# Kernel tuning notes

Measured on AMD Instinct MI355X. Metric: run time of the kernel, lower is better.

The kernel has to match this reference:

```python
import jax, jax.numpy as jnp
import numpy as np

EPS = 1e-08

def setup_inputs() -> dict:
    key = jax.random.key(0)
    k1, k2 = jax.random.split(key)
    h = jax.random.normal(k1, (4096, 512), dtype=jnp.float32)   # [B, D]
    A = jax.random.normal(k2, (32768, 512), dtype=jnp.float32)  # [K, D]
    return {"h": h, "A": A}

def _l2_normalize(x, eps=EPS):
    # matches torch F.normalize(p=2): x / max(||x||, eps)
    n = jnp.sqrt(jnp.sum(x * x, axis=-1, keepdims=True))
    return x / jnp.maximum(n, eps)

def reference(h, A):
    # cosine metric: normalize both, matmul, argmax over K
    h_n = _l2_normalize(h)                      # [B, D]
    A_n = _l2_normalize(A)                      # [K, D]
    scores = jnp.einsum('bd,kd->bk', h_n, A_n)  # [B, K]
    idx = jnp.argmax(scores, axis=1, keepdims=True)  # [B, 1] int
    return idx
```

## Files before the change

kernel.cpp:

```cpp
#include <hip/hip_runtime.h>
#include <stdint.h>


#define DIM 512
#define B_ROWS 4096
#define K_ROWS 32768
#define BT 128
#define KT 128
#define NKT (K_ROWS / KT)
#define KSLOTS 32
#define NCHUNK 4
#define QSCALE (127.0f / 0.26f)

typedef __attribute__((ext_vector_type(4))) float fx4;
typedef __attribute__((ext_vector_type(4))) int int4v;
typedef unsigned long long u64;

__device__ __forceinline__ uint32_t ford(float s) {
    uint32_t u = __float_as_uint(s);
    return u ^ ((uint32_t)((int32_t)u >> 31) | 0x80000000u);
}
__device__ __forceinline__ u64 umax64(u64 a, u64 b) { return a > b ? a : b; }
__device__ __forceinline__ u64 umin64(u64 a, u64 b) { return a < b ? a : b; }
__device__ __forceinline__ uint32_t umax32(uint32_t a, uint32_t b) { return a > b ? a : b; }
__device__ __forceinline__ uint32_t umin32(uint32_t a, uint32_t b) { return a < b ? a : b; }

__device__ __forceinline__ int q8(float x, float qs) {
    int v = __float2int_rn(x * qs);
    return v < -127 ? -127 : (v > 127 ? 127 : v);
}

__global__ __launch_bounds__(256) void prep_kernel(const float* __restrict__ A,
                                                   const float* __restrict__ h,
                                                   char* __restrict__ a8,
                                                   char* __restrict__ h8,
                                                   float* __restrict__ rn) {
    const int lane = threadIdx.x & 63, wid = threadIdx.x >> 6;
    const bool isA = blockIdx.x < 8192;
    const int row = (isA ? blockIdx.x : blockIdx.x - 8192) * 4 + wid;
    const float* src = (isA ? A : h) + (size_t)row * DIM;
    char* dst = (isA ? a8 : h8) + (size_t)row * DIM;

    const fx4* p = (const fx4*)src;
    fx4 a = p[lane * 2], b = p[lane * 2 + 1];
    float ss = a[0]*a[0] + a[1]*a[1] + a[2]*a[2] + a[3]*a[3]
             + b[0]*b[0] + b[1]*b[1] + b[2]*b[2] + b[3]*b[3];
    #pragma unroll
    for (int off = 32; off > 0; off >>= 1) ss += __shfl_xor(ss, off, 64);
    float r = 1.0f / fmaxf(sqrtf(ss), 1e-8f);
    if (isA && lane == 0) rn[row] = r;

    float qs = r * QSCALE;
    int v0 = q8(a[0], qs), v1 = q8(a[1], qs), v2 = q8(a[2], qs), v3 = q8(a[3], qs);
    int v4 = q8(b[0], qs), v5 = q8(b[1], qs), v6 = q8(b[2], qs), v7 = q8(b[3], qs);
    uint32_t lo = (uint32_t)(v0 & 255) | ((uint32_t)(v1 & 255) << 8)
                | ((uint32_t)(v2 & 255) << 16) | ((uint32_t)(v3 & 255) << 24);
    uint32_t hi = (uint32_t)(v4 & 255) | ((uint32_t)(v5 & 255) << 8)
                | ((uint32_t)(v6 & 255) << 16) | ((uint32_t)(v7 & 255) << 24);
    *reinterpret_cast<uint2*>(dst + lane * 8) = make_uint2(lo, hi);
}

typedef __attribute__((address_space(3))) uint32_t lds_u32;
typedef __attribute__((address_space(1))) const uint32_t g_u32;

__global__ __launch_bounds__(256, 3) void score_kernel(
    const char* __restrict__ h8, const char* __restrict__ a8,
    u64* __restrict__ cand)
{
    __shared__ __attribute__((aligned(16))) char smem[33792];
    char* hf = smem;
    char* af = smem + 16384;

    const int t = threadIdx.x, lane = t & 63, wid = t >> 6;
    const int wm = wid >> 1, wn = wid & 1;
    const int lr = lane & 15, q = lane >> 4;
    const int btile = blockIdx.x >> 5, kslot = blockIdx.x & 31;
    const int b0 = btile * BT;

    const int srow = lane >> 3;
    const int scol = (lane & 7) ^ srow;
    const int s7 = lr & 7;
    const int sw0 = (q ^ s7) * 16;
    const int sw1 = ((4 + q) ^ s7) * 16;

    const char* hsrc = h8 + (size_t)b0 * DIM;

    uint32_t v1[16], v2[16];
    #pragma unroll
    for (int s = 0; s < 16; s++) { v1[s] = 0u; v2[s] = 0u; }

    int it = 0;
    #pragma unroll 1
    for (int kt = kslot; kt < NKT; kt += KSLOTS, it++) {
        const int k0 = kt * KT;
        const char* asrc = a8 + (size_t)k0 * DIM;

        int4v acc[4][4];
        #pragma unroll
        for (int mi = 0; mi < 4; mi++)
            #pragma unroll
            for (int ni = 0; ni < 4; ni++)
                acc[mi][ni] = (int4v){0, 0, 0, 0};

        #pragma unroll 1
        for (int dc = 0; dc < NCHUNK; dc++) {
            __syncthreads();
            #pragma unroll
            for (int i = 0; i < 4; i++) {
                int issue = wid * 4 + i;
                size_t roff = (size_t)(issue * 8 + srow) * DIM + dc * 128 + scol * 16;
                __builtin_amdgcn_global_load_lds((g_u32*)(hsrc + roff),
                    (lds_u32*)(hf + issue * 1024), 16, 0, 0);
                __builtin_amdgcn_global_load_lds((g_u32*)(asrc + roff),
                    (lds_u32*)(af + issue * 1024), 16, 0, 0);
            }
            __syncthreads();

            int4v af0[4], af1[4];
            #pragma unroll
            for (int ni = 0; ni < 4; ni++) {
                const char* base = af + (wn * 64 + ni * 16 + lr) * 128;
                af0[ni] = *reinterpret_cast<const int4v*>(base + sw0);
                af1[ni] = *reinterpret_cast<const int4v*>(base + sw1);
            }
            #pragma unroll
            for (int mi = 0; mi < 4; mi++) {
                const char* base = hf + (wm * 64 + mi * 16 + lr) * 128;
                int4v h0 = *reinterpret_cast<const int4v*>(base + sw0);
                int4v h1 = *reinterpret_cast<const int4v*>(base + sw1);
                #pragma unroll
                for (int ni = 0; ni < 4; ni++) {
                    acc[mi][ni] = __builtin_amdgcn_mfma_i32_16x16x64_i8(h0, af0[ni], acc[mi][ni], 0, 0, 0);
                    acc[mi][ni] = __builtin_amdgcn_mfma_i32_16x16x64_i8(h1, af1[ni], acc[mi][ni], 0, 0, 0);
                }
            }
        }

        const uint32_t metabase = (uint32_t)(it << 2);
        #pragma unroll
        for (int mi = 0; mi < 4; mi++)
            #pragma unroll
            for (int ni = 0; ni < 4; ni++) {
                const uint32_t meta = metabase | (uint32_t)ni;
                #pragma unroll
                for (int r = 0; r < 4; r++) {
                    uint32_t ord = (uint32_t)acc[mi][ni][r] ^ 0x80000000u;
                    uint32_t pk = (ord & 0xFFFFFFC0u) | meta;
                    int s = mi * 4 + r;
                    uint32_t lo = umin32(v1[s], pk);
                    v1[s] = umax32(v1[s], pk);
                    v2[s] = umax32(v2[s], lo);
                }
            }
    }

    uint32_t* cl = (uint32_t*)smem;
    u64 g1 = 0, g2 = 0, g3 = 0;
    for (int pass = 0; pass < 2; pass++) {
        __syncthreads();
        #pragma unroll
        for (int s = 0; s < 16; s++) {
            int mi = s >> 2, r = s & 3;
            int row_local = wm * 64 + mi * 16 + q * 4 + r;
            cl[row_local * 33 + wn * 16 + lr] = pass ? v2[s] : v1[s];
        }
        __syncthreads();
        if (t < BT) {
            #pragma unroll 4
            for (int j = 0; j < 32; j++) {
                uint32_t pv = cl[t * 33 + j];
                uint32_t meta = pv & 63u;
                int k = (kslot + (int)(meta >> 2) * KSLOTS) * KT
                      + (j >> 4) * 64 + (int)(meta & 3u) * 16 + (j & 15);
                u64 e = ((u64)(pv & 0xFFFFFFC0u) << 32) | (u64)(~(uint32_t)k);
                u64 t1 = umax64(g1, e), t2 = umin64(g1, e);
                g3 = umax64(g3, umin64(g2, t2));
                g2 = umax64(g2, t2);
                g1 = t1;
            }
        }
    }
    if (t < BT) {
        size_t base = ((size_t)(b0 + t) * KSLOTS + kslot) * 3;
        cand[base] = g1;
        cand[base + 1] = g2;
        cand[base + 2] = g3;
    }
}

__global__ __launch_bounds__(256) void refine_kernel(
    const float* __restrict__ h, const float* __restrict__ A,
    const float* __restrict__ rn, const u64* __restrict__ cand,
    int* __restrict__ out)
{
    const int t = threadIdx.x, lane = t & 63, wid = t >> 6;
    const int row = blockIdx.x * 4 + wid;
    const u64* cr = cand + (size_t)row * (KSLOTS * 3);
    u64 x0 = cr[lane];
    u64 x1 = (lane < KSLOTS * 3 - 64) ? cr[64 + lane] : 0ULL;

    u64 sel[8];
    #pragma unroll
    for (int j = 0; j < 8; j++) {
        u64 v = umax64(x0, x1);
        #pragma unroll
        for (int m = 32; m >= 1; m >>= 1) v = umax64(v, __shfl_xor(v, m, 64));
        sel[j] = v;
        if (x0 == v) x0 = 0;
        else if (x1 == v) x1 = 0;
    }

    const fx4* hp = reinterpret_cast<const fx4*>(h + (size_t)row * DIM);
    fx4 h0 = hp[lane * 2], h1 = hp[lane * 2 + 1];

    u64 best = 0;
    #pragma unroll
    for (int j = 0; j < 8; j++) {
        uint32_t kg = ~(uint32_t)sel[j];
        const fx4* ap = reinterpret_cast<const fx4*>(A + (size_t)kg * DIM);
        fx4 a0 = ap[lane * 2], a1 = ap[lane * 2 + 1];
        float s = h0[0]*a0[0] + h0[1]*a0[1] + h0[2]*a0[2] + h0[3]*a0[3]
                + h1[0]*a1[0] + h1[1]*a1[1] + h1[2]*a1[2] + h1[3]*a1[3];
        #pragma unroll
        for (int m = 32; m >= 1; m >>= 1) s += __shfl_xor(s, m, 64);
        s *= rn[kg];
        u64 pk = ((u64)ford(s) << 32) | (u64)(~kg);
        best = umax64(best, pk);
    }
    if (lane == 0) out[row] = (int)(~(uint32_t)best);
}

extern "C" void kernel_launch(void* const* d_in, const int* in_sizes, int n_in,
                              void* d_out, int out_size, void* d_ws, size_t ws_size,
                              hipStream_t stream) {
    const float* h = (const float*)d_in[0];
    const float* A = (const float*)d_in[1];
    int* out = (int*)d_out;

    char* w = (char*)d_ws;
    char* a8 = w;
    char* h8 = w + (size_t)K_ROWS * DIM;
    float* rn = (float*)(w + (size_t)(K_ROWS + B_ROWS) * DIM);
    u64* cand = (u64*)(w + (size_t)(K_ROWS + B_ROWS) * DIM
                         + (size_t)K_ROWS * sizeof(float));

    prep_kernel<<<8192 + 1024, 256, 0, stream>>>(A, h, a8, h8, rn);
    score_kernel<<<32 * KSLOTS, 256, 0, stream>>>(h8, a8, cand);
    refine_kernel<<<B_ROWS / 4, 256, 0, stream>>>(h, A, rn, cand, out);
}
```

Baseline: 203.9 us.

## Double-buffer LDS tiles to overlap global loads with int8 MFMA compute

Replaces the single LDS tile buffer with two 32 KB buffers. The next D-chunk is now issued via global_load_lds into the alternate buffer while the current chunk is consumed by MFMAs, and one barrier per chunk replaces two. LDS use doubles to 64 KB, so launch bounds drop from 3 to 2 blocks per CU, trading occupancy for latency hiding. The loop is hardcoded to 8 k-tile iterations per slot.

```diff
diff --git a/kernel.cpp b/kernel.cpp
--- a/kernel.cpp
+++ b/kernel.cpp
@@ -63,13 +63,11 @@
 typedef __attribute__((address_space(3))) uint32_t lds_u32;
 typedef __attribute__((address_space(1))) const uint32_t g_u32;
 
-__global__ __launch_bounds__(256, 3) void score_kernel(
+__global__ __launch_bounds__(256, 2) void score_kernel(
     const char* __restrict__ h8, const char* __restrict__ a8,
     u64* __restrict__ cand)
 {
-    __shared__ __attribute__((aligned(16))) char smem[33792];
-    char* hf = smem;
-    char* af = smem + 16384;
+    __shared__ __attribute__((aligned(16))) char smem[65536];
 
     const int t = threadIdx.x, lane = t & 63, wid = t >> 6;
     const int wm = wid >> 1, wn = wid & 1;
@@ -89,12 +87,28 @@
     #pragma unroll
     for (int s = 0; s < 16; s++) { v1[s] = 0u; v2[s] = 0u; }
 
-    int it = 0;
+    auto stage = [&](int cc, int buf) {
+        const int kt = kslot + (cc >> 2) * KSLOTS;
+        const int dcc = cc & 3;
+        const char* asrc = a8 + (size_t)(kt * KT) * DIM;
+        char* hb = smem + buf * 32768;
+        char* ab = hb + 16384;
+        #pragma unroll
+        for (int i = 0; i < 4; i++) {
+            int issue = wid * 4 + i;
+            size_t roff = (size_t)(issue * 8 + srow) * DIM + dcc * 128 + scol * 16;
+            __builtin_amdgcn_global_load_lds((g_u32*)(hsrc + roff),
+                (lds_u32*)(hb + issue * 1024), 16, 0, 0);
+            __builtin_amdgcn_global_load_lds((g_u32*)(asrc + roff),
+                (lds_u32*)(ab + issue * 1024), 16, 0, 0);
+        }
+    };
+
+    stage(0, 0);
+    __syncthreads();
+
     #pragma unroll 1
-    for (int kt = kslot; kt < NKT; kt += KSLOTS, it++) {
-        const int k0 = kt * KT;
-        const char* asrc = a8 + (size_t)k0 * DIM;
-
+    for (int it = 0; it < 8; it++) {
         int4v acc[4][4];
         #pragma unroll
         for (int mi = 0; mi < 4; mi++)
@@ -102,19 +116,13 @@
             for (int ni = 0; ni < 4; ni++)
                 acc[mi][ni] = (int4v){0, 0, 0, 0};
 
-        #pragma unroll 1
-        for (int dc = 0; dc < NCHUNK; dc++) {
-            __syncthreads();
-            #pragma unroll
-            for (int i = 0; i < 4; i++) {
-                int issue = wid * 4 + i;
-                size_t roff = (size_t)(issue * 8 + srow) * DIM + dc * 128 + scol * 16;
-                __builtin_amdgcn_global_load_lds((g_u32*)(hsrc + roff),
-                    (lds_u32*)(hf + issue * 1024), 16, 0, 0);
-                __builtin_amdgcn_global_load_lds((g_u32*)(asrc + roff),
-                    (lds_u32*)(af + issue * 1024), 16, 0, 0);
-            }
-            __syncthreads();
+        #pragma unroll
+        for (int dc = 0; dc < 4; dc++) {
+            const int c = it * 4 + dc;
+            if (dc < 3 || it < 7) stage(c + 1, (dc & 1) ^ 1);
+
+            const char* hf = smem + (dc & 1) * 32768;
+            const char* af = hf + 16384;
 
             int4v af0[4], af1[4];
             #pragma unroll
@@ -134,24 +142,28 @@
                     acc[mi][ni] = __builtin_amdgcn_mfma_i32_16x16x64_i8(h1, af1[ni], acc[mi][ni], 0, 0, 0);
                 }
             }
-        }
-
-        const uint32_t metabase = (uint32_t)(it << 2);
-        #pragma unroll
-        for (int mi = 0; mi < 4; mi++)
-            #pragma unroll
-            for (int ni = 0; ni < 4; ni++) {
-                const uint32_t meta = metabase | (uint32_t)ni;
+
+            if (dc == 3) {
+                const uint32_t metabase = (uint32_t)(it << 2);
                 #pragma unroll
-                for (int r = 0; r < 4; r++) {
-                    uint32_t ord = (uint32_t)acc[mi][ni][r] ^ 0x80000000u;
-                    uint32_t pk = (ord & 0xFFFFFFC0u) | meta;
-                    int s = mi * 4 + r;
-                    uint32_t lo = umin32(v1[s], pk);
-                    v1[s] = umax32(v1[s], pk);
-                    v2[s] = umax32(v2[s], lo);
-                }
-            }
+                for (int mi = 0; mi < 4; mi++)
+                    #pragma unroll
+                    for (int ni = 0; ni < 4; ni++) {
+                        const uint32_t meta = metabase | (uint32_t)ni;
+                        #pragma unroll
+                        for (int r = 0; r < 4; r++) {
+                            uint32_t ord = (uint32_t)acc[mi][ni][r] ^ 0x80000000u;
+                            uint32_t pk = (ord & 0xFFFFFFC0u) | meta;
+                            int s = mi * 4 + r;
+                            uint32_t lo = umin32(v1[s], pk);
+                            v1[s] = umax32(v1[s], pk);
+                            v2[s] = umax32(v2[s], lo);
+                        }
+                    }
+            }
+
+            __syncthreads();
+        }
     }
 
     uint32_t* cl = (uint32_t*)smem;
```

After: 198.7 us. 2.6% less time.
